# Performance work log

Measured on AMD Instinct MI355X. Metric: run time of the kernel, lower is better.

## Reference

```python
import jax, jax.numpy as jnp
import numpy as np

H = 64   # hidden_dim
L = 3    # num_layers
N = 1024 # num nodes


def silu(x):
    return x * jax.nn.sigmoid(x)


def setup_inputs() -> dict:
    key = jax.random.key(0)
    ks = jax.random.split(key, 32)
    rn = lambda k, shape: jax.random.normal(k, shape, dtype=jnp.float32) * 0.05
    inp = {}
    inp["pos_noisy"] = jax.random.normal(ks[0], (N, 3), dtype=jnp.float32)
    adj = (jax.random.uniform(ks[1], (N, N)) > 0.5).astype(jnp.float32)
    adj = jnp.triu(adj, 1)
    inp["adj_noisy"] = adj + adj.T  # symmetric binary, zero diagonal
    inp["node_mask"] = jnp.ones((N,), jnp.float32)
    inp["t"] = 50
    # time_mlp: Linear(H,H) -> SiLU -> Linear(H,H)
    inp["tw1"] = rn(ks[2], (H, H)); inp["tb1"] = rn(ks[3], (H,))
    inp["tw2"] = rn(ks[4], (H, H)); inp["tb2"] = rn(ks[5], (H,))
    # pos_encoder: Linear(3,H)
    inp["pw"] = rn(ks[6], (3, H)); inp["pb"] = rn(ks[7], (H,))
    # per-layer edge MLPs: Linear(4,H) -> SiLU -> Linear(H,H), stacked over L
    inp["ew1"] = rn(ks[8], (L, 4, H)); inp["eb1"] = rn(ks[9], (L, H))
    inp["ew2"] = rn(ks[10], (L, H, H)); inp["eb2"] = rn(ks[11], (L, H))
    # per-layer mp layers: Linear(3H, H)
    inp["mw"] = rn(ks[12], (L, 3 * H, H)); inp["mb"] = rn(ks[13], (L, H))
    # adj_head: Linear(2H,H) -> SiLU -> Linear(H,1)
    inp["aw1"] = rn(ks[14], (2 * H, H)); inp["ab1"] = rn(ks[15], (H,))
    inp["aw2"] = rn(ks[16], (H, 1)); inp["ab2"] = rn(ks[17], (1,))
    # pos_head: Linear(2H,H) -> SiLU -> Linear(H,3)
    inp["hw1"] = rn(ks[18], (2 * H, H)); inp["hb1"] = rn(ks[19], (H,))
    inp["hw2"] = rn(ks[20], (H, 3)); inp["hb2"] = rn(ks[21], (3,))
    return inp


def reference(pos_noisy, adj_noisy, node_mask, t,
              tw1, tb1, tw2, tb2, pw, pb,
              ew1, eb1, ew2, eb2, mw, mb,
              aw1, ab1, aw2, ab2, hw1, hb1, hw2, hb2):
    n = pos_noisy.shape[0]
    half = H // 2
    # sinusoidal timestep embedding
    freqs = jnp.exp(jnp.arange(half, dtype=jnp.float32) * (-np.log(10000.0) / (half - 1)))
    tf = jnp.float32(t) * freqs
    te = jnp.concatenate([jnp.sin(tf), jnp.cos(tf)])            # (H,)
    te = silu(te @ tw1 + tb1) @ tw2 + tb2                        # time_mlp -> (H,)
    te_b = jnp.broadcast_to(te, (n, H))

    h = pos_noisy @ pw + pb + te[None, :]                        # (N,H)

    # relative geometry is constant across layers (pos does not change in the loop)
    rel = pos_noisy[:, None, :] - pos_noisy[None, :, :]          # (N,N,3)
    dist = jnp.linalg.norm(rel, axis=-1, keepdims=True)          # (N,N,1)
    ef_in = jnp.concatenate([rel, dist], axis=-1)                # (N,N,4)

    for l in range(L):
        ef = silu(ef_in @ ew1[l] + eb1[l]) @ ew2[l] + eb2[l]     # (N,N,H) edge features
        msg = jnp.einsum('ij,ijh->ih', adj_noisy, ef) + h        # adjacency-weighted sum over j
        h = silu(jnp.concatenate([h, msg, te_b], axis=-1) @ mw[l] + mb[l])

    # adj_head(cat(h_i, h_j)) without materializing (N,N,2H): split first linear
    hi = h @ aw1[:H]                                             # (N,H)
    hj = h @ aw1[H:]                                             # (N,H)
    ah = silu(hi[:, None, :] + hj[None, :, :] + ab1)             # (N,N,H)
    logits = jnp.squeeze(ah @ aw2 + ab2, -1)                     # (N,N)
    logits = (logits + logits.T) * 0.5
    adj_pred = jax.nn.sigmoid(logits) * node_mask[None, :] * node_mask[:, None]

    eps = silu(jnp.concatenate([h, te_b], axis=-1) @ hw1 + hb1) @ hw2 + hb2
    eps_pred = eps * node_mask[:, None]
    return adj_pred, eps_pred
```

## Files before the change

### kernel.cpp

```cpp
#include <hip/hip_runtime.h>
#include <math.h>

#define NN 1024
#define HD 64
#define NL 3

#define WHI 0
#define WHJ (NN*HD)

__device__ __forceinline__ float fsilu(float x) {
    float e = __expf(-x);
    return x * __builtin_amdgcn_rcpf(1.0f + e);
}
__device__ __forceinline__ float fsigmoid(float x) {
    float e = __expf(-x);
    return __builtin_amdgcn_rcpf(1.0f + e);
}

__global__ __launch_bounds__(512, 6) void k_main(
    const float* __restrict__ pos, const float* __restrict__ adj,
    const float* __restrict__ nmask, const int* __restrict__ tp,
    const float* __restrict__ tw1, const float* __restrict__ tb1,
    const float* __restrict__ tw2, const float* __restrict__ tb2,
    const float* __restrict__ pw, const float* __restrict__ pb,
    const float* __restrict__ ew1, const float* __restrict__ eb1,
    const float* __restrict__ ew2, const float* __restrict__ eb2,
    const float* __restrict__ mw,  const float* __restrict__ mb,
    const float* __restrict__ aw1,
    const float* __restrict__ hw1, const float* __restrict__ hb1,
    const float* __restrict__ hw2, const float* __restrict__ hb2,
    float* __restrict__ ws, float* __restrict__ out)
{
    __shared__ float4 s_ef[NN];
    __shared__ float  s_red[2048];
    __shared__ float  s_cat[3*HD];
    __shared__ float  s_s[HD];
    __shared__ float  s_eu[HD];
    __shared__ int    s_nnz;

    const int i = blockIdx.x;
    const int t = threadIdx.x;
    const int lane = t & 63;

    if (t == 0) s_nnz = 0;
    __syncthreads();

    const float pix = pos[3*i+0], piy = pos[3*i+1], piz = pos[3*i+2];
    for (int base = 0; base < NN; base += 512) {
        const int j = base + t;
        const bool nz = (adj[i*NN + j] != 0.0f);
        const unsigned long long m = __ballot(nz);
        int wb = 0;
        if (lane == 0) wb = atomicAdd(&s_nnz, __popcll(m));
        wb = __shfl(wb, 0);
        if (nz) {
            const int k = wb + __popcll(m & ((1ull << lane) - 1ull));
            const float dx = pix - pos[3*j+0];
            const float dy = piy - pos[3*j+1];
            const float dz = piz - pos[3*j+2];
            s_ef[k] = make_float4(dx, dy, dz, sqrtf(dx*dx + dy*dy + dz*dz));
        }
    }
    if (t < HD) {
        const float tv = (float)(*tp);
        const float fr = expf((float)(t & 31) * (-logf(10000.0f) / 31.0f));
        const float ang = tv * fr;
        s_red[t] = (t < 32) ? sinf(ang) : cosf(ang);
    }
    __syncthreads();
    const int nnz = s_nnz;
    const float deg = (float)nnz;
    if (t < HD) {
        float a = tb1[t];
        #pragma unroll 8
        for (int k = 0; k < HD; ++k) a = fmaf(s_red[k], tw1[k*HD + t], a);
        s_red[HD + t] = fsilu(a);
    }
    __syncthreads();
    if (t < HD) {
        float te = tb2[t];
        #pragma unroll 8
        for (int k = 0; k < HD; ++k) te = fmaf(s_red[HD + k], tw2[k*HD + t], te);
        s_cat[2*HD + t] = te;
        float a = pb[t] + te;
        a = fmaf(pix, pw[0*HD + t], a);
        a = fmaf(piy, pw[1*HD + t], a);
        a = fmaf(piz, pw[2*HD + t], a);
        s_cat[t] = a;
    }
    __syncthreads();

    const int jj = t >> 4;
    const int hb = (t & 15) << 2;
    const int q  = t >> 6;
    const int h2 = t & 63;

    for (int l = 0; l < NL; ++l) {
        float w0[4], w1[4], w2[4], w3[4], bb[4];
        #pragma unroll
        for (int r = 0; r < 4; ++r) {
            w0[r] = ew1[(l*4 + 0)*HD + hb + r];
            w1[r] = ew1[(l*4 + 1)*HD + hb + r];
            w2[r] = ew1[(l*4 + 2)*HD + hb + r];
            w3[r] = ew1[(l*4 + 3)*HD + hb + r];
            bb[r] = eb1[l*HD + hb + r];
        }
        float acc[4] = {0.f, 0.f, 0.f, 0.f};
        for (int k = jj; k < nnz; k += 32) {
            const float4 ef = s_ef[k];
            #pragma unroll
            for (int r = 0; r < 4; ++r) {
                float g = fmaf(ef.x, w0[r], bb[r]);
                g = fmaf(ef.y, w1[r], g);
                g = fmaf(ef.z, w2[r], g);
                g = fmaf(ef.w, w3[r], g);
                acc[r] += fsilu(g);
            }
        }
        *reinterpret_cast<float4*>(&s_red[jj*HD + hb]) =
            make_float4(acc[0], acc[1], acc[2], acc[3]);
        __syncthreads();
        if (t < HD) {
            float s = 0.0f;
            #pragma unroll
            for (int ww = 0; ww < 32; ++ww) s += s_red[ww*HD + t];
            s_s[t] = s;
        }
        __syncthreads();
        {
            float pm = 0.0f;
            #pragma unroll
            for (int kk = 0; kk < 8; ++kk) {
                const int k = q*8 + kk;
                pm = fmaf(s_s[k], ew2[(l*HD + k)*HD + h2], pm);
            }
            s_red[q*HD + h2] = pm;
        }
        __syncthreads();
        if (t < HD) {
            float m = 0.0f;
            #pragma unroll
            for (int w = 0; w < 8; ++w) m += s_red[w*HD + t];
            m = fmaf(deg, eb2[l*HD + t], m);
            s_cat[HD + t] = m + s_cat[t];
        }
        __syncthreads();
        {
            float ph = 0.0f;
            #pragma unroll
            for (int kk = 0; kk < 24; ++kk) {
                const int row = q*24 + kk;
                ph = fmaf(s_cat[row], mw[(l*3*HD + row)*HD + h2], ph);
            }
            s_red[q*HD + h2] = ph;
        }
        __syncthreads();
        if (t < HD) {
            float a = mb[l*HD + t];
            #pragma unroll
            for (int w = 0; w < 8; ++w) a += s_red[w*HD + t];
            s_cat[t] = fsilu(a);
        }
        __syncthreads();
    }

    if (t < HD) {
        float a = hb1[t];
        #pragma unroll 8
        for (int k = 0; k < HD; ++k) a = fmaf(s_cat[k], hw1[k*HD + t], a);
        #pragma unroll 8
        for (int k = 0; k < HD; ++k) a = fmaf(s_cat[2*HD + k], hw1[(HD + k)*HD + t], a);
        s_eu[t] = fsilu(a);
    } else if (t < 2*HD) {
        const int c = t - HD;
        float a1 = 0.f, a2 = 0.f;
        #pragma unroll 8
        for (int k = 0; k < HD; ++k) {
            a1 = fmaf(s_cat[k], aw1[k*HD + c], a1);
            a2 = fmaf(s_cat[k], aw1[(HD + k)*HD + c], a2);
        }
        ws[WHI + i*HD + c] = a1;
        ws[WHJ + i*HD + c] = a2;
    }
    __syncthreads();
    if (t < 3) {
        float e = hb2[t];
        for (int k = 0; k < HD; ++k) e = fmaf(s_eu[k], hw2[k*3 + t], e);
        out[NN*NN + i*3 + t] = e * nmask[i];
    }
}

__global__ __launch_bounds__(256) void k_adj(
    const float* __restrict__ ws, const float* __restrict__ nmask,
    const float* __restrict__ ab1, const float* __restrict__ aw2,
    const float* __restrict__ ab2, float* __restrict__ out)
{
    __shared__ float4 s_hiI[16*17], s_hjJ[16*17], s_hiJ[16*17], s_hjI[16*17];
    __shared__ float4 s_ab[16], s_w[16];
    __shared__ float s_L1[16][17], s_L2[16][17];
    const int T = NN / 16;
    const int b = blockIdx.x;
    int I = (int)((2.0*T + 1.0 -
                   sqrt((2.0*T + 1.0)*(2.0*T + 1.0) - 8.0*(double)b)) * 0.5);
    if (I < 0) I = 0; if (I > T-1) I = T-1;
    while (I+1 <= T-1 && ((I+1)*T - ((I+1)*I)/2) <= b) ++I;
    while (I > 0 && (I*T - (I*(I-1))/2) > b) --I;
    const int J = I + (b - (I*T - (I*(I-1))/2));
    const int I0 = I*16, J0 = J*16;
    const int t = threadIdx.x;
    const float* hi = ws + WHI;
    const float* hj = ws + WHJ;
    if (t < 16) { s_ab[t] = ((const float4*)ab1)[t]; s_w[t] = ((const float4*)aw2)[t]; }
    for (int idx = t; idx < 4*16*16; idx += 256) {
        const int arr = idx >> 8, rem = idx & 255, r = rem >> 4, qq = rem & 15;
        const float* src = (arr == 0 || arr == 2) ? hi : hj;
        const int rowt = (arr == 0 || arr == 3) ? I0 : J0;
        const float4 v = *reinterpret_cast<const float4*>(src + (rowt + r)*HD + qq*4);
        float4* dst = (arr == 0) ? s_hiI : (arr == 1) ? s_hjJ
                     : (arr == 2) ? s_hiJ : s_hjI;
        dst[r*17 + qq] = v;
    }
    __syncthreads();
    const int r = t >> 4, c = t & 15;
    float l1 = 0.f, l2 = 0.f;
    #pragma unroll
    for (int hq = 0; hq < 16; ++hq) {
        const float4 aI = s_hiI[r*17 + hq];
        const float4 bJ = s_hjJ[c*17 + hq];
        const float4 aJ = s_hiJ[r*17 + hq];
        const float4 bI = s_hjI[c*17 + hq];
        const float4 ab = s_ab[hq];
        const float4 w  = s_w[hq];
        l1 += fsilu(aI.x + bJ.x + ab.x)*w.x + fsilu(aI.y + bJ.y + ab.y)*w.y
            + fsilu(aI.z + bJ.z + ab.z)*w.z + fsilu(aI.w + bJ.w + ab.w)*w.w;
        l2 += fsilu(aJ.x + bI.x + ab.x)*w.x + fsilu(aJ.y + bI.y + ab.y)*w.y
            + fsilu(aJ.z + bI.z + ab.z)*w.z + fsilu(aJ.w + bI.w + ab.w)*w.w;
    }
    const float b2 = ab2[0];
    s_L1[r][c] = l1 + b2;
    s_L2[r][c] = l2 + b2;
    __syncthreads();
    const float v1 = 0.5f*(s_L1[r][c] + s_L2[c][r]);
    const float v2 = 0.5f*(s_L2[r][c] + s_L1[c][r]);
    const int gi1 = I0 + r, gj1 = J0 + c;
    out[gi1*NN + gj1] = fsigmoid(v1) * nmask[gi1] * nmask[gj1];
    const int gi2 = J0 + r, gj2 = I0 + c;
    out[gi2*NN + gj2] = fsigmoid(v2) * nmask[gi2] * nmask[gj2];
}

extern "C" void kernel_launch(void* const* d_in, const int* in_sizes, int n_in,
                              void* d_out, int out_size, void* d_ws, size_t ws_size,
                              hipStream_t stream) {
    const float* pos   = (const float*)d_in[0];
    const float* adjp  = (const float*)d_in[1];
    const float* nmask = (const float*)d_in[2];
    const int*   tp    = (const int*)d_in[3];
    const float* tw1   = (const float*)d_in[4];
    const float* tb1   = (const float*)d_in[5];
    const float* tw2   = (const float*)d_in[6];
    const float* tb2   = (const float*)d_in[7];
    const float* pw    = (const float*)d_in[8];
    const float* pb    = (const float*)d_in[9];
    const float* ew1   = (const float*)d_in[10];
    const float* eb1   = (const float*)d_in[11];
    const float* ew2   = (const float*)d_in[12];
    const float* eb2   = (const float*)d_in[13];
    const float* mw    = (const float*)d_in[14];
    const float* mb    = (const float*)d_in[15];
    const float* aw1   = (const float*)d_in[16];
    const float* ab1   = (const float*)d_in[17];
    const float* aw2   = (const float*)d_in[18];
    const float* ab2   = (const float*)d_in[19];
    const float* hw1   = (const float*)d_in[20];
    const float* hb1   = (const float*)d_in[21];
    const float* hw2   = (const float*)d_in[22];
    const float* hb2   = (const float*)d_in[23];
    float* ws  = (float*)d_ws;
    float* out = (float*)d_out;

    hipLaunchKernelGGL(k_main, dim3(NN), dim3(512), 0, stream,
                       pos, adjp, nmask, tp, tw1, tb1, tw2, tb2, pw, pb,
                       ew1, eb1, ew2, eb2, mw, mb, aw1, hw1, hb1, hw2, hb2,
                       ws, out);
    hipLaunchKernelGGL(k_adj, dim3((NN/16)*((NN/16)+1)/2), dim3(256), 0, stream,
                       ws, nmask, ab1, aw2, ab2, out);
}
```

Baseline: 174.9 us.

## Precompute weight-only terms and fold ew2 into message weights; batch edge MLP across layers

Adds a small pre-kernel that computes the time embedding, its projections through mw and hw1, the eb2 contribution, and the combined matrices [mw_h+mw_msg; ew2·mw_msg] for each layer. The main kernel then evaluates all three layers' first edge-MLP stage in a single pass over the nonzero edges and applies one fused matvec per layer, which removes the separate ew2 matvec and several barriers. ab1 is folded into hj so the adjacency kernel skips an add per element. The cost is an extra launch and workspace traffic, more registers for the fused edge loop, and a reordered floating-point sum.

Result: faster. 166.4 us (-4.9%).

```diff
diff --git a/kernel.cpp b/kernel.cpp
--- a/kernel.cpp
+++ b/kernel.cpp
@@ -5,8 +5,13 @@
 #define HD 64
 #define NL 3
 
-#define WHI 0
-#define WHJ (NN*HD)
+#define WTE 0
+#define WTC 64
+#define WEC 256
+#define WCV 320
+#define WW  512
+#define WHI (512 + 3*128*64)
+#define WHJ (WHI + NN*HD)
 
 __device__ __forceinline__ float fsilu(float x) {
     float e = __expf(-x);
@@ -17,25 +22,100 @@
     return __builtin_amdgcn_rcpf(1.0f + e);
 }
 
+__global__ __launch_bounds__(256) void k_pre(
+    const int* __restrict__ tp,
+    const float* __restrict__ tw1, const float* __restrict__ tb1,
+    const float* __restrict__ tw2, const float* __restrict__ tb2,
+    const float* __restrict__ ew2, const float* __restrict__ eb2,
+    const float* __restrict__ mw,  const float* __restrict__ mb,
+    const float* __restrict__ hw1, const float* __restrict__ hb1,
+    float* __restrict__ ws)
+{
+    const int b = blockIdx.x, t = threadIdx.x;
+    if (b == 0) {
+        __shared__ float raw[HD], x1[HD], te[HD];
+        if (t < HD) {
+            const float tv = (float)(*tp);
+            const float fr = __expf((float)(t & 31) * (-logf(10000.0f) / 31.0f));
+            const float ang = tv * fr;
+            raw[t] = (t < 32) ? sinf(ang) : cosf(ang);
+        }
+        __syncthreads();
+        if (t < HD) {
+            float a = tb1[t];
+            #pragma unroll 8
+            for (int k = 0; k < HD; ++k) a = fmaf(raw[k], tw1[k*HD + t], a);
+            x1[t] = fsilu(a);
+        }
+        __syncthreads();
+        if (t < HD) {
+            float a = tb2[t];
+            #pragma unroll 8
+            for (int k = 0; k < HD; ++k) a = fmaf(x1[k], tw2[k*HD + t], a);
+            te[t] = a;
+            ws[WTE + t] = a;
+        }
+        __syncthreads();
+        if (t < 192) {
+            const int l = t >> 6, h = t & 63;
+            float a = mb[l*HD + h];
+            float c = 0.0f;
+            #pragma unroll 8
+            for (int k = 0; k < HD; ++k) {
+                a = fmaf(te[k],          mw[(l*3*HD + 2*HD + k)*HD + h], a);
+                c = fmaf(eb2[l*HD + k],  mw[(l*3*HD +   HD + k)*HD + h], c);
+            }
+            ws[WTC + t] = a;
+            ws[WCV + t] = c;
+        } else {
+            const int h = t - 192;
+            float a = hb1[h];
+            #pragma unroll 8
+            for (int k = 0; k < HD; ++k) a = fmaf(te[k], hw1[(HD + k)*HD + h], a);
+            ws[WEC + h] = a;
+        }
+    } else {
+        const int l = b - 1;
+        __shared__ float s_w2[HD*HD];
+        __shared__ float s_mm[HD*HD];
+        for (int o = t; o < HD*HD; o += 256) {
+            const int r = o >> 6, h = o & 63;
+            s_w2[o] = ew2[l*HD*HD + o];
+            const float mm = mw[(l*3*HD + HD + r)*HD + h];
+            s_mm[o] = mm;
+            ws[WW + l*128*HD + o] = mw[(l*3*HD + r)*HD + h] + mm;
+        }
+        __syncthreads();
+        const int h = t & 63, r0 = t >> 6;
+        float acc[16];
+        #pragma unroll
+        for (int ri = 0; ri < 16; ++ri) acc[ri] = 0.0f;
+        for (int k = 0; k < HD; ++k) {
+            const float mv = s_mm[k*HD + h];
+            #pragma unroll
+            for (int ri = 0; ri < 16; ++ri)
+                acc[ri] = fmaf(s_w2[(r0*16 + ri)*HD + k], mv, acc[ri]);
+        }
+        #pragma unroll
+        for (int ri = 0; ri < 16; ++ri)
+            ws[WW + l*128*HD + (HD + r0*16 + ri)*HD + h] = acc[ri];
+    }
+}
+
 __global__ __launch_bounds__(512, 6) void k_main(
     const float* __restrict__ pos, const float* __restrict__ adj,
-    const float* __restrict__ nmask, const int* __restrict__ tp,
-    const float* __restrict__ tw1, const float* __restrict__ tb1,
-    const float* __restrict__ tw2, const float* __restrict__ tb2,
+    const float* __restrict__ nmask,
     const float* __restrict__ pw, const float* __restrict__ pb,
     const float* __restrict__ ew1, const float* __restrict__ eb1,
-    const float* __restrict__ ew2, const float* __restrict__ eb2,
-    const float* __restrict__ mw,  const float* __restrict__ mb,
-    const float* __restrict__ aw1,
-    const float* __restrict__ hw1, const float* __restrict__ hb1,
+    const float* __restrict__ aw1, const float* __restrict__ ab1,
+    const float* __restrict__ hw1,
     const float* __restrict__ hw2, const float* __restrict__ hb2,
     float* __restrict__ ws, float* __restrict__ out)
 {
     __shared__ float4 s_ef[NN];
-    __shared__ float  s_red[2048];
-    __shared__ float  s_cat[3*HD];
-    __shared__ float  s_s[HD];
-    __shared__ float  s_eu[HD];
+    __shared__ float  s_red[16*NL*HD];
+    __shared__ float  s_s[NL*HD];
+    __shared__ float  s_h[HD], s_eu[HD];
     __shared__ int    s_nnz;
 
     const int i = blockIdx.x;
@@ -62,125 +142,97 @@
         }
     }
     if (t < HD) {
-        const float tv = (float)(*tp);
-        const float fr = expf((float)(t & 31) * (-logf(10000.0f) / 31.0f));
-        const float ang = tv * fr;
-        s_red[t] = (t < 32) ? sinf(ang) : cosf(ang);
-    }
-    __syncthreads();
-    const int nnz = s_nnz;
-    const float deg = (float)nnz;
-    if (t < HD) {
-        float a = tb1[t];
-        #pragma unroll 8
-        for (int k = 0; k < HD; ++k) a = fmaf(s_red[k], tw1[k*HD + t], a);
-        s_red[HD + t] = fsilu(a);
-    }
-    __syncthreads();
-    if (t < HD) {
-        float te = tb2[t];
-        #pragma unroll 8
-        for (int k = 0; k < HD; ++k) te = fmaf(s_red[HD + k], tw2[k*HD + t], te);
-        s_cat[2*HD + t] = te;
-        float a = pb[t] + te;
+        float a = pb[t] + ws[WTE + t];
         a = fmaf(pix, pw[0*HD + t], a);
         a = fmaf(piy, pw[1*HD + t], a);
         a = fmaf(piz, pw[2*HD + t], a);
-        s_cat[t] = a;
-    }
-    __syncthreads();
-
-    const int jj = t >> 4;
-    const int hb = (t & 15) << 2;
-    const int q  = t >> 6;
-    const int h2 = t & 63;
-
+        s_h[t] = a;
+    }
+    __syncthreads();
+    const int nnz = s_nnz;
+    const float deg = (float)nnz;
+
+    const int jj = t >> 5;
+    const int hp = t & 31;
+    float w[NL][2][4], bb[NL][2], acc[NL][2];
+    #pragma unroll
+    for (int l = 0; l < NL; ++l)
+        #pragma unroll
+        for (int c = 0; c < 2; ++c) {
+            const int hc = hp + 32*c;
+            #pragma unroll
+            for (int m = 0; m < 4; ++m) w[l][c][m] = ew1[(l*4 + m)*HD + hc];
+            bb[l][c] = eb1[l*HD + hc];
+            acc[l][c] = 0.0f;
+        }
+    for (int k = jj; k < nnz; k += 16) {
+        const float4 ef = s_ef[k];
+        #pragma unroll
+        for (int l = 0; l < NL; ++l)
+            #pragma unroll
+            for (int c = 0; c < 2; ++c) {
+                float g = fmaf(ef.x, w[l][c][0], bb[l][c]);
+                g = fmaf(ef.y, w[l][c][1], g);
+                g = fmaf(ef.z, w[l][c][2], g);
+                g = fmaf(ef.w, w[l][c][3], g);
+                acc[l][c] += fsilu(g);
+            }
+    }
+    #pragma unroll
+    for (int l = 0; l < NL; ++l)
+        #pragma unroll
+        for (int c = 0; c < 2; ++c)
+            s_red[(l*16 + jj)*HD + hp + 32*c] = acc[l][c];
+    __syncthreads();
+    if (t < NL*HD) {
+        const int l = t >> 6, h = t & 63;
+        float s = 0.0f;
+        #pragma unroll
+        for (int g = 0; g < 16; ++g) s += s_red[(l*16 + g)*HD + h];
+        s_s[l*HD + h] = s;
+    }
+    __syncthreads();
+
+    const int q = t >> 6, h2 = t & 63;
     for (int l = 0; l < NL; ++l) {
-        float w0[4], w1[4], w2[4], w3[4], bb[4];
-        #pragma unroll
-        for (int r = 0; r < 4; ++r) {
-            w0[r] = ew1[(l*4 + 0)*HD + hb + r];
-            w1[r] = ew1[(l*4 + 1)*HD + hb + r];
-            w2[r] = ew1[(l*4 + 2)*HD + hb + r];
-            w3[r] = ew1[(l*4 + 3)*HD + hb + r];
-            bb[r] = eb1[l*HD + hb + r];
-        }
-        float acc[4] = {0.f, 0.f, 0.f, 0.f};
-        for (int k = jj; k < nnz; k += 32) {
-            const float4 ef = s_ef[k];
+        const float* Wl = ws + WW + l*128*HD;
+        float pm = 0.0f;
+        #pragma unroll
+        for (int kk = 0; kk < 16; ++kk) {
+            const int row = q*16 + kk;
+            const float x = (row < HD) ? s_h[row] : s_s[l*HD + row - HD];
+            pm = fmaf(x, Wl[row*HD + h2], pm);
+        }
+        s_red[q*HD + h2] = pm;
+        __syncthreads();
+        if (t < HD) {
+            float a = ws[WTC + l*HD + t];
+            a = fmaf(deg, ws[WCV + l*HD + t], a);
             #pragma unroll
-            for (int r = 0; r < 4; ++r) {
-                float g = fmaf(ef.x, w0[r], bb[r]);
-                g = fmaf(ef.y, w1[r], g);
-                g = fmaf(ef.z, w2[r], g);
-                g = fmaf(ef.w, w3[r], g);
-                acc[r] += fsilu(g);
-            }
-        }
-        *reinterpret_cast<float4*>(&s_red[jj*HD + hb]) =
-            make_float4(acc[0], acc[1], acc[2], acc[3]);
-        __syncthreads();
-        if (t < HD) {
-            float s = 0.0f;
-            #pragma unroll
-            for (int ww = 0; ww < 32; ++ww) s += s_red[ww*HD + t];
-            s_s[t] = s;
-        }
-        __syncthreads();
-        {
-            float pm = 0.0f;
-            #pragma unroll
-            for (int kk = 0; kk < 8; ++kk) {
-                const int k = q*8 + kk;
-                pm = fmaf(s_s[k], ew2[(l*HD + k)*HD + h2], pm);
-            }
-            s_red[q*HD + h2] = pm;
-        }
-        __syncthreads();
-        if (t < HD) {
-            float m = 0.0f;
-            #pragma unroll
-            for (int w = 0; w < 8; ++w) m += s_red[w*HD + t];
-            m = fmaf(deg, eb2[l*HD + t], m);
-            s_cat[HD + t] = m + s_cat[t];
-        }
-        __syncthreads();
-        {
-            float ph = 0.0f;
-            #pragma unroll
-            for (int kk = 0; kk < 24; ++kk) {
-                const int row = q*24 + kk;
-                ph = fmaf(s_cat[row], mw[(l*3*HD + row)*HD + h2], ph);
-            }
-            s_red[q*HD + h2] = ph;
-        }
-        __syncthreads();
-        if (t < HD) {
-            float a = mb[l*HD + t];
-            #pragma unroll
-            for (int w = 0; w < 8; ++w) a += s_red[w*HD + t];
-            s_cat[t] = fsilu(a);
-        }
-        __syncthreads();
-    }
-
-    if (t < HD) {
-        float a = hb1[t];
-        #pragma unroll 8
-        for (int k = 0; k < HD; ++k) a = fmaf(s_cat[k], hw1[k*HD + t], a);
-        #pragma unroll 8
-        for (int k = 0; k < HD; ++k) a = fmaf(s_cat[2*HD + k], hw1[(HD + k)*HD + t], a);
-        s_eu[t] = fsilu(a);
-    } else if (t < 2*HD) {
-        const int c = t - HD;
-        float a1 = 0.f, a2 = 0.f;
-        #pragma unroll 8
-        for (int k = 0; k < HD; ++k) {
-            a1 = fmaf(s_cat[k], aw1[k*HD + c], a1);
-            a2 = fmaf(s_cat[k], aw1[(HD + k)*HD + c], a2);
-        }
-        ws[WHI + i*HD + c] = a1;
-        ws[WHJ + i*HD + c] = a2;
+            for (int g = 0; g < 8; ++g) a += s_red[g*HD + t];
+            s_h[t] = fsilu(a);
+        }
+        __syncthreads();
+    }
+
+    if (t < 192) {
+        const int sel = t >> 6, col = t & 63;
+        if (sel == 0) {
+            float a = ws[WEC + col];
+            #pragma unroll 8
+            for (int k = 0; k < HD; ++k) a = fmaf(s_h[k], hw1[k*HD + col], a);
+            s_eu[col] = fsilu(a);
+        } else if (sel == 1) {
+            float a = 0.0f;
+            #pragma unroll 8
+            for (int k = 0; k < HD; ++k) a = fmaf(s_h[k], aw1[k*HD + col], a);
+            ws[WHI + i*HD + col] = a;
+        } else {
+            float a = ab1[col];
+            #pragma unroll 8
+            for (int k = 0; k < HD; ++k) a = fmaf(s_h[k], aw1[(HD + k)*HD + col], a);
+            ws[WHJ + i*HD + col] = a;
+        }
     }
     __syncthreads();
     if (t < 3) {
@@ -192,11 +244,11 @@
 
 __global__ __launch_bounds__(256) void k_adj(
     const float* __restrict__ ws, const float* __restrict__ nmask,
-    const float* __restrict__ ab1, const float* __restrict__ aw2,
-    const float* __restrict__ ab2, float* __restrict__ out)
+    const float* __restrict__ aw2, const float* __restrict__ ab2,
+    float* __restrict__ out)
 {
     __shared__ float4 s_hiI[16*17], s_hjJ[16*17], s_hiJ[16*17], s_hjI[16*17];
-    __shared__ float4 s_ab[16], s_w[16];
+    __shared__ float4 s_w[16];
     __shared__ float s_L1[16][17], s_L2[16][17];
     const int T = NN / 16;
     const int b = blockIdx.x;
@@ -210,7 +262,7 @@
     const int t = threadIdx.x;
     const float* hi = ws + WHI;
     const float* hj = ws + WHJ;
-    if (t < 16) { s_ab[t] = ((const float4*)ab1)[t]; s_w[t] = ((const float4*)aw2)[t]; }
+    if (t < 16) s_w[t] = ((const float4*)aw2)[t];
     for (int idx = t; idx < 4*16*16; idx += 256) {
         const int arr = idx >> 8, rem = idx & 255, r = rem >> 4, qq = rem & 15;
         const float* src = (arr == 0 || arr == 2) ? hi : hj;
@@ -229,12 +281,11 @@
         const float4 bJ = s_hjJ[c*17 + hq];
         const float4 aJ = s_hiJ[r*17 + hq];
         const float4 bI = s_hjI[c*17 + hq];
-        const float4 ab = s_ab[hq];
         const float4 w  = s_w[hq];
-        l1 += fsilu(aI.x + bJ.x + ab.x)*w.x + fsilu(aI.y + bJ.y + ab.y)*w.y
-            + fsilu(aI.z + bJ.z + ab.z)*w.z + fsilu(aI.w + bJ.w + ab.w)*w.w;
-        l2 += fsilu(aJ.x + bI.x + ab.x)*w.x + fsilu(aJ.y + bI.y + ab.y)*w.y
-            + fsilu(aJ.z + bI.z + ab.z)*w.z + fsilu(aJ.w + bI.w + ab.w)*w.w;
+        l1 += fsilu(aI.x + bJ.x)*w.x + fsilu(aI.y + bJ.y)*w.y
+            + fsilu(aI.z + bJ.z)*w.z + fsilu(aI.w + bJ.w)*w.w;
+        l2 += fsilu(aJ.x + bI.x)*w.x + fsilu(aJ.y + bI.y)*w.y
+            + fsilu(aJ.z + bI.z)*w.z + fsilu(aJ.w + bI.w)*w.w;
     }
     const float b2 = ab2[0];
     s_L1[r][c] = l1 + b2;
@@ -278,10 +329,11 @@
     float* ws  = (float*)d_ws;
     float* out = (float*)d_out;
 
+    hipLaunchKernelGGL(k_pre, dim3(1 + NL), dim3(256), 0, stream,
+                       tp, tw1, tb1, tw2, tb2, ew2, eb2, mw, mb, hw1, hb1, ws);
     hipLaunchKernelGGL(k_main, dim3(NN), dim3(512), 0, stream,
-                       pos, adjp, nmask, tp, tw1, tb1, tw2, tb2, pw, pb,
-                       ew1, eb1, ew2, eb2, mw, mb, aw1, hw1, hb1, hw2, hb2,
-                       ws, out);
+                       pos, adjp, nmask, pw, pb, ew1, eb1, aw1, ab1,
+                       hw1, hw2, hb2, ws, out);
     hipLaunchKernelGGL(k_adj, dim3((NN/16)*((NN/16)+1)/2), dim3(256), 0, stream,
-                       ws, nmask, ab1, aw2, ab2, out);
-}
+                       ws, nmask, aw2, ab2, out);
+}
```
